# Kernel optimization log

Measured on AMD Instinct MI355X. Metric: run time of the kernel, lower is better.

Reference implementation:

```python
import jax, jax.numpy as jnp
import numpy as np

B, N, D = 262144, 3, 64

def setup_inputs() -> dict:
    key = jax.random.key(0)
    k = jax.random.split(key, 6)
    lim1 = 1.0 / np.sqrt(2 * D)
    lim2 = 1.0 / np.sqrt(D)
    nodes = jax.random.normal(k[0], (B, N, D), dtype=jnp.float32)
    W1 = jax.random.uniform(k[1], (2 * D, D), jnp.float32, -lim1, lim1)
    b1 = jax.random.uniform(k[2], (D,), jnp.float32, -lim1, lim1)
    W2 = jax.random.uniform(k[3], (D, D), jnp.float32, -lim2, lim2)
    b2 = jax.random.uniform(k[4], (D,), jnp.float32, -lim2, lim2)
    edge_attn = jnp.array([[0.0, 1.5, 0.5], [1.5, 0.0, 0.8], [0.3, 0.8, 0.0]], dtype=jnp.float32)
    return {"nodes": nodes, "W1": W1, "b1": b1, "W2": W2, "b2": b2, "edge_attn": edge_attn}

def reference(nodes, W1, b1, W2, b2, edge_attn):
    b, n, d = nodes.shape
    # pairwise concat: (B, N, N, 2D) with ni varying over axis 1, nj over axis 2
    ni = jnp.broadcast_to(nodes[:, :, None, :], (b, n, n, d))
    nj = jnp.broadcast_to(nodes[:, None, :, :], (b, n, n, d))
    x = jnp.concatenate([ni, nj], axis=-1)            # (B,N,N,2D)
    h = jax.nn.gelu(x @ W1 + b1, approximate=False)   # torch nn.GELU default = exact erf
    msg = h @ W2 + b2                                 # (B,N,N,D)
    attn = jax.nn.softmax(edge_attn, axis=-1)         # (N,N)
    agg = jnp.einsum('ij,bijd->bid', attn, msg)       # weighted sum over j
    return agg
```

## Files before the change

### kernel.cpp

```cpp
#include <hip/hip_runtime.h>
#include <math.h>

typedef __attribute__((ext_vector_type(8))) short bf16x8;
typedef __attribute__((ext_vector_type(4))) float f32x4;

#define WSTR 68

__device__ __forceinline__ unsigned short f2b(float f) {
    union { float f; unsigned int u; } x; x.f = f;
    unsigned int r = x.u + 0x7FFFu + ((x.u >> 16) & 1u);
    return (unsigned short)(r >> 16);
}

__device__ __forceinline__ float gelu_t(float x) {
    float x2 = x * x;
    float z  = x * fmaf(0.10294324f, x2, 2.3022082f);
    float e  = __builtin_amdgcn_exp2f(z);
    float r  = __builtin_amdgcn_rcpf(1.0f + e);
    return fmaf(x, -r, x);
}

__global__ void prep_k(const float* __restrict__ W1, const float* __restrict__ W2,
                       const float* __restrict__ ea, unsigned short* __restrict__ w1t,
                       unsigned short* __restrict__ w2t, float* __restrict__ attn)
{
    int gid = blockIdx.x * 256 + threadIdx.x;
    if (gid < 128 * 64) {
        int n = gid >> 6, k = gid & 63;
        float v = (n < 64) ? W1[k * 64 + n] : W1[(64 + k) * 64 + (n - 64)];
        w1t[gid] = f2b(v);
    } else if (gid < 12288) {
        int idx = gid - 8192;
        int n = idx >> 6, k = idx & 63;
        w2t[idx] = f2b(W2[k * 64 + n]);
    }
    if (gid < 9) {
        int i = gid / 3, j = gid % 3;
        float e0 = ea[i*3+0], e1 = ea[i*3+1], e2 = ea[i*3+2];
        float mx = fmaxf(e0, fmaxf(e1, e2));
        float d = expf(e0-mx) + expf(e1-mx) + expf(e2-mx);
        attn[gid] = expf(ea[i*3+j] - mx) / d;
    }
}

__global__ __launch_bounds__(256, 3)
void edge_mfma3(const float* __restrict__ nodes,
                const unsigned short* __restrict__ w1t,
                const unsigned short* __restrict__ w2t,
                const float* __restrict__ attn9,
                const float* __restrict__ b1,
                const float* __restrict__ b2,
                float* __restrict__ out)
{
    __shared__ __align__(16) unsigned short Gs[4 * 16 * WSTR];

    const int t = threadIdx.x;
    const int lane = t & 63, wave = t >> 6;
    const int q = lane >> 4, r16 = lane & 15;
    unsigned short* Gw = Gs + wave * 16 * WSTR;

    const int bA = r16 >> 2;
    const int iA = ((r16 & 3) == 3) ? 0 : (r16 & 3);

    bf16x8 w1f[8][2], w2f[4][2];
    #pragma unroll
    for (int nt = 0; nt < 8; ++nt)
        #pragma unroll
        for (int ks = 0; ks < 2; ++ks)
            w1f[nt][ks] = *(const bf16x8*)&w1t[(nt*16 + r16) * 64 + ks*32 + q*8];
    #pragma unroll
    for (int nt = 0; nt < 4; ++nt)
        #pragma unroll
        for (int ks = 0; ks < 2; ++ks)
            w2f[nt][ks] = *(const bf16x8*)&w2t[(nt*16 + r16) * 64 + ks*32 + q*8];

    float aw[3][3];
    #pragma unroll
    for (int i = 0; i < 3; ++i)
        #pragma unroll
        for (int j = 0; j < 3; ++j) aw[i][j] = attn9[i*3+j];
    float b1c[4], b2c[4];
    #pragma unroll
    for (int nt = 0; nt < 4; ++nt) { b1c[nt] = b1[nt*16 + r16]; b2c[nt] = b2[nt*16 + r16]; }

    const int batch0 = blockIdx.x * 64 + wave * 16;

    #pragma unroll
    for (int mt = 0; mt < 4; ++mt) {
        const long rowA = ((long)(batch0 + mt*4 + bA)) * 3 + iA;
        const f32x4* xp = (const f32x4*)(nodes + rowA * 64 + q * 8);
        f32x4 x0 = xp[0], x1 = xp[1], x2v = xp[8], x3 = xp[9];
        bf16x8 afr0, afr1;
        #pragma unroll
        for (int e = 0; e < 4; ++e) {
            afr0[e]   = (short)f2b(x0[e]);  afr0[4+e] = (short)f2b(x1[e]);
            afr1[e]   = (short)f2b(x2v[e]); afr1[4+e] = (short)f2b(x3[e]);
        }

        #pragma unroll
        for (int nt = 0; nt < 4; ++nt) {
            f32x4 z = {0.f, 0.f, 0.f, 0.f};
            z = __builtin_amdgcn_mfma_f32_16x16x32_bf16(afr0, w1f[nt][0], z, 0, 0, 0);
            z = __builtin_amdgcn_mfma_f32_16x16x32_bf16(afr1, w1f[nt][1], z, 0, 0, 0);
            f32x4 y = {0.f, 0.f, 0.f, 0.f};
            y = __builtin_amdgcn_mfma_f32_16x16x32_bf16(afr0, w1f[nt+4][0], y, 0, 0, 0);
            y = __builtin_amdgcn_mfma_f32_16x16x32_bf16(afr1, w1f[nt+4][1], y, 0, 0, 0);

            float u0 = z[0] + b1c[nt], u1 = z[1] + b1c[nt], u2 = z[2] + b1c[nt];
            float gg0 = 0.f, gg1 = 0.f, gg2 = 0.f;
            #pragma unroll
            for (int j = 0; j < 3; ++j) {
                float vj = y[j];
                float gl0 = gelu_t(u0 + vj);
                float gl1 = gelu_t(u1 + vj);
                float gl2 = gelu_t(u2 + vj);
                gg0 = fmaf(aw[0][j], gl0, gg0);
                gg1 = fmaf(aw[1][j], gl1, gg1);
                gg2 = fmaf(aw[2][j], gl2, gg2);
            }
            Gw[(q*4 + 0) * WSTR + nt*16 + r16] = f2b(gg0);
            Gw[(q*4 + 1) * WSTR + nt*16 + r16] = f2b(gg1);
            Gw[(q*4 + 2) * WSTR + nt*16 + r16] = f2b(gg2);
        }

        bf16x8 gfr0 = *(const bf16x8*)&Gw[r16 * WSTR + q*8];
        bf16x8 gfr1 = *(const bf16x8*)&Gw[r16 * WSTR + 32 + q*8];
        #pragma unroll
        for (int nt = 0; nt < 4; ++nt) {
            f32x4 acc = {0.f, 0.f, 0.f, 0.f};
            acc = __builtin_amdgcn_mfma_f32_16x16x32_bf16(gfr0, w2f[nt][0], acc, 0, 0, 0);
            acc = __builtin_amdgcn_mfma_f32_16x16x32_bf16(gfr1, w2f[nt][1], acc, 0, 0, 0);
            float* op = out + ((long)(batch0 + mt*4 + q) * 3) * 64 + nt*16 + r16;
            #pragma unroll
            for (int r = 0; r < 3; ++r)
                __builtin_nontemporal_store(acc[r] + b2c[nt], op + r * 64);
        }
    }
}

extern "C" void kernel_launch(void* const* d_in, const int* in_sizes, int n_in,
                              void* d_out, int out_size, void* d_ws, size_t ws_size,
                              hipStream_t stream)
{
    const float* nodes = (const float*)d_in[0];
    const float* W1    = (const float*)d_in[1];
    const float* b1    = (const float*)d_in[2];
    const float* W2    = (const float*)d_in[3];
    const float* b2    = (const float*)d_in[4];
    const float* ea    = (const float*)d_in[5];
    float* out = (float*)d_out;

    unsigned short* w1t = (unsigned short*)d_ws;
    unsigned short* w2t = w1t + 8192;
    float* attn = (float*)(w2t + 4096);

    prep_k<<<48, 256, 0, stream>>>(W1, W2, ea, w1t, w2t, attn);

    const int groups = (out_size / 64) / 3 / 64;
    edge_mfma3<<<groups, 256, 0, stream>>>(nodes, w1t, w2t, attn, b1, b2, out);
}
```

Baseline: 98.75 us.

## Loop over batch tiles with next-tile prefetch and vectorized transposed output stores

Each block now processes eight 16-batch tiles in a loop instead of one fixed 64-batch chunk. While the current tile computes, the next tile's node rows are loaded into registers, and the grid is halved. The second MFMA swaps its operands so each lane holds four consecutive output columns, which turns the scalar output stores into 16-byte vector nontemporal stores with a vector b2 load. The attention weights are also made wave-uniform via readfirstlane. In exchange the prefetch costs extra registers and there are fewer blocks to hide latency, in a kernel that is bound by streaming memory traffic.

```diff
diff --git a/kernel.cpp b/kernel.cpp
--- a/kernel.cpp
+++ b/kernel.cpp
@@ -4,7 +4,8 @@
 typedef __attribute__((ext_vector_type(8))) short bf16x8;
 typedef __attribute__((ext_vector_type(4))) float f32x4;
 
-#define WSTR 68
+#define WSTR  68
+#define ITERS 8
 
 __device__ __forceinline__ unsigned short f2b(float f) {
     union { float f; unsigned int u; } x; x.f = f;
@@ -44,7 +45,7 @@
 }
 
 __global__ __launch_bounds__(256, 3)
-void edge_mfma3(const float* __restrict__ nodes,
+void edge_mfma4(const float* __restrict__ nodes,
                 const unsigned short* __restrict__ w1t,
                 const unsigned short* __restrict__ w2t,
                 const float* __restrict__ attn9,
@@ -60,7 +61,8 @@
     unsigned short* Gw = Gs + wave * 16 * WSTR;
 
     const int bA = r16 >> 2;
-    const int iA = ((r16 & 3) == 3) ? 0 : (r16 & 3);
+    const int iA = r16 & 3;
+    const int iAr = (iA == 3) ? 0 : iA;
 
     bf16x8 w1f[8][2], w2f[4][2];
     #pragma unroll
@@ -74,27 +76,38 @@
         for (int ks = 0; ks < 2; ++ks)
             w2f[nt][ks] = *(const bf16x8*)&w2t[(nt*16 + r16) * 64 + ks*32 + q*8];
 
-    float aw[3][3];
+    float aw[9];
     #pragma unroll
-    for (int i = 0; i < 3; ++i)
-        #pragma unroll
-        for (int j = 0; j < 3; ++j) aw[i][j] = attn9[i*3+j];
-    float b1c[4], b2c[4];
+    for (int i = 0; i < 9; ++i) {
+        union { float f; int u; } c; c.f = attn9[i];
+        c.u = __builtin_amdgcn_readfirstlane(c.u);
+        aw[i] = c.f;
+    }
+    float b1c[4];
     #pragma unroll
-    for (int nt = 0; nt < 4; ++nt) { b1c[nt] = b1[nt*16 + r16]; b2c[nt] = b2[nt*16 + r16]; }
+    for (int nt = 0; nt < 4; ++nt) b1c[nt] = b1[nt*16 + r16];
 
-    const int batch0 = blockIdx.x * 64 + wave * 16;
+    const long batch0 = (long)blockIdx.x * (ITERS * 16) + wave * 4 + bA;
+    const float* xlane = nodes + (batch0 * 3 + iAr) * 64 + q * 8;
+    float*       olane = out   + (batch0 * 3 + iA ) * 64 + q * 4;
 
-    #pragma unroll
-    for (int mt = 0; mt < 4; ++mt) {
-        const long rowA = ((long)(batch0 + mt*4 + bA)) * 3 + iA;
-        const f32x4* xp = (const f32x4*)(nodes + rowA * 64 + q * 8);
-        f32x4 x0 = xp[0], x1 = xp[1], x2v = xp[8], x3 = xp[9];
+    f32x4 c0 = *(const f32x4*)(xlane);
+    f32x4 c1 = *(const f32x4*)(xlane + 4);
+    f32x4 c2 = *(const f32x4*)(xlane + 32);
+    f32x4 c3 = *(const f32x4*)(xlane + 36);
+
+    for (int it = 0; it < ITERS; ++it) {
+        const float* xn = xlane + (long)((it + 1 < ITERS) ? it + 1 : it) * 3072;
+        f32x4 n0 = *(const f32x4*)(xn);
+        f32x4 n1 = *(const f32x4*)(xn + 4);
+        f32x4 n2 = *(const f32x4*)(xn + 32);
+        f32x4 n3 = *(const f32x4*)(xn + 36);
+
         bf16x8 afr0, afr1;
         #pragma unroll
         for (int e = 0; e < 4; ++e) {
-            afr0[e]   = (short)f2b(x0[e]);  afr0[4+e] = (short)f2b(x1[e]);
-            afr1[e]   = (short)f2b(x2v[e]); afr1[4+e] = (short)f2b(x3[e]);
+            afr0[e]   = (short)f2b(c0[e]); afr0[4+e] = (short)f2b(c1[e]);
+            afr1[e]   = (short)f2b(c2[e]); afr1[4+e] = (short)f2b(c3[e]);
         }
 
         #pragma unroll
@@ -114,9 +127,9 @@
                 float gl0 = gelu_t(u0 + vj);
                 float gl1 = gelu_t(u1 + vj);
                 float gl2 = gelu_t(u2 + vj);
-                gg0 = fmaf(aw[0][j], gl0, gg0);
-                gg1 = fmaf(aw[1][j], gl1, gg1);
-                gg2 = fmaf(aw[2][j], gl2, gg2);
+                gg0 = fmaf(aw[0*3+j], gl0, gg0);
+                gg1 = fmaf(aw[1*3+j], gl1, gg1);
+                gg2 = fmaf(aw[2*3+j], gl2, gg2);
             }
             Gw[(q*4 + 0) * WSTR + nt*16 + r16] = f2b(gg0);
             Gw[(q*4 + 1) * WSTR + nt*16 + r16] = f2b(gg1);
@@ -128,13 +141,17 @@
         #pragma unroll
         for (int nt = 0; nt < 4; ++nt) {
             f32x4 acc = {0.f, 0.f, 0.f, 0.f};
-            acc = __builtin_amdgcn_mfma_f32_16x16x32_bf16(gfr0, w2f[nt][0], acc, 0, 0, 0);
-            acc = __builtin_amdgcn_mfma_f32_16x16x32_bf16(gfr1, w2f[nt][1], acc, 0, 0, 0);
-            float* op = out + ((long)(batch0 + mt*4 + q) * 3) * 64 + nt*16 + r16;
-            #pragma unroll
-            for (int r = 0; r < 3; ++r)
-                __builtin_nontemporal_store(acc[r] + b2c[nt], op + r * 64);
+            acc = __builtin_amdgcn_mfma_f32_16x16x32_bf16(w2f[nt][0], gfr0, acc, 0, 0, 0);
+            acc = __builtin_amdgcn_mfma_f32_16x16x32_bf16(w2f[nt][1], gfr1, acc, 0, 0, 0);
+            if (iA != 3) {
+                f32x4 b2v = *(const f32x4*)(b2 + nt*16 + q*4);
+                f32x4 o = acc + b2v;
+                __builtin_nontemporal_store(o, (f32x4*)(olane + (long)it * 3072 + nt * 16));
+            }
         }
+
+        c0 = n0; c1 = n1; c2 = n2; c3 = n3;
+        xlane += 0;
     }
 }
 
@@ -156,6 +173,7 @@
 
     prep_k<<<48, 256, 0, stream>>>(W1, W2, ea, w1t, w2t, attn);
 
-    const int groups = (out_size / 64) / 3 / 64;
-    edge_mfma3<<<groups, 256, 0, stream>>>(nodes, w1t, w2t, attn, b1, b2, out);
+    const int batches = (out_size / 64) / 3;
+    const int blocks = batches / (ITERS * 16);
+    edge_mfma4<<<blocks, 256, 0, stream>>>(nodes, w1t, w2t, attn, b1, b2, out);
 }
```

Result: slower. 106.8 us (+8.2%).
